# Optimization experiments

Measured on AMD Instinct MI355X. Metric: run time of the kernel, lower is better.

Reference implementation:

```python
import jax, jax.numpy as jnp
import numpy as np

B, N, CH, DIM, SLOTS, ITERS, HID = 32, 4096, 256, 256, 11, 3, 512
EPS_ATTN = 1e-8
LN_EPS = 1e-3


def _ln(x, g, b):
    m = jnp.mean(x, axis=-1, keepdims=True)
    v = jnp.mean((x - m) ** 2, axis=-1, keepdims=True)
    return (x - m) * jax.lax.rsqrt(v + LN_EPS) * g + b


def setup_inputs() -> dict:
    key = jax.random.key(0)
    ks = jax.random.split(key, 16)
    s = lambda d: 1.0 / np.sqrt(d)
    return {
        "inputs": jax.random.normal(ks[0], (B, N, CH), jnp.float32),
        "noise": jax.random.normal(ks[1], (B, SLOTS, DIM), jnp.float32),
        "slots_mu": jax.random.uniform(ks[2], (1, 1, DIM), jnp.float32, -0.15, 0.15),
        "slots_log_sigma": jax.random.uniform(ks[3], (1, 1, DIM), jnp.float32, -0.15, 0.15),
        "Wq": jax.random.normal(ks[4], (DIM, DIM), jnp.float32) * s(DIM),
        "Wk": jax.random.normal(ks[5], (DIM, CH), jnp.float32) * s(CH),
        "Wv": jax.random.normal(ks[6], (DIM, CH), jnp.float32) * s(CH),
        "W_ih": jax.random.normal(ks[7], (3 * DIM, DIM), jnp.float32) * s(DIM),
        "W_hh": jax.random.normal(ks[8], (3 * DIM, DIM), jnp.float32) * s(DIM),
        "b_ih": jnp.zeros((3 * DIM,), jnp.float32),
        "b_hh": jnp.zeros((3 * DIM,), jnp.float32),
        "W1": jax.random.normal(ks[9], (HID, DIM), jnp.float32) * s(DIM),
        "b1": jnp.zeros((HID,), jnp.float32),
        "W2": jax.random.normal(ks[10], (DIM, HID), jnp.float32) * s(HID),
        "b2": jnp.zeros((DIM,), jnp.float32),
        "g_in": jnp.ones((CH,), jnp.float32), "be_in": jnp.zeros((CH,), jnp.float32),
        "g_sl": jnp.ones((DIM,), jnp.float32), "be_sl": jnp.zeros((DIM,), jnp.float32),
        "g_ff": jnp.ones((DIM,), jnp.float32), "be_ff": jnp.zeros((DIM,), jnp.float32),
    }


def reference(inputs, noise, slots_mu, slots_log_sigma, Wq, Wk, Wv, W_ih, W_hh,
              b_ih, b_hh, W1, b1, W2, b2, g_in, be_in, g_sl, be_sl, g_ff, be_ff):
    scale = DIM ** -0.5
    # reparameterized slot init: Normal(mu, exp(log_sigma))
    slots = slots_mu + jnp.exp(slots_log_sigma) * noise  # (B, S, D)
    x = _ln(inputs, g_in, be_in)
    k = jnp.einsum('bnc,dc->bnd', x, Wk)  # (B, N, D)
    v = jnp.einsum('bnc,dc->bnd', x, Wv)

    def gru(u, h):
        gi = u @ W_ih.T + b_ih
        gh = h @ W_hh.T + b_hh
        i_r, i_z, i_n = jnp.split(gi, 3, axis=-1)
        h_r, h_z, h_n = jnp.split(gh, 3, axis=-1)
        r = jax.nn.sigmoid(i_r + h_r)
        z = jax.nn.sigmoid(i_z + h_z)
        n = jnp.tanh(i_n + r * h_n)
        return (1.0 - z) * n + z * h

    for _ in range(ITERS):
        slots_prev = slots
        q = jnp.einsum('bid,ed->bie', _ln(slots, g_sl, be_sl), Wq)
        dots = jnp.einsum('bid,bjd->bij', q, k) * scale  # (B, S, N)
        attn = jax.nn.softmax(dots, axis=1) + EPS_ATTN   # competitive over slots
        attn = attn / jnp.sum(attn, axis=-1, keepdims=True)
        updates = jnp.einsum('bjd,bij->bid', v, attn)    # (B, S, D)
        slots = gru(updates.reshape(-1, DIM), slots_prev.reshape(-1, DIM)).reshape(B, -1, DIM)
        h = jax.nn.relu(_ln(slots, g_ff, be_ff) @ W1.T + b1)
        slots = slots + h @ W2.T + b2
    return slots
```

## Files before the change

### kernel.cpp

```cpp
#include <hip/hip_runtime.h>
#include <hip/hip_bf16.h>
#include <math.h>

typedef __bf16 bf16;
typedef __bf16 bf16x4 __attribute__((ext_vector_type(4)));
typedef __bf16 bf16x8 __attribute__((ext_vector_type(8)));
typedef float  f32x4  __attribute__((ext_vector_type(4)));

#define DEVI static __device__ __forceinline__

constexpr int B_ = 32, N_ = 4096, NS_ = 11, SP_ = 16, ITERS_ = 3;
constexpr int P_ = 32;
constexpr float LN_EPS_ = 1e-3f;
constexpr float EPS_ATTN_ = 1e-8f;

DEVI f32x4 mfma16(bf16x8 a, bf16x8 b, f32x4 c) {
  return __builtin_amdgcn_mfma_f32_16x16x32_bf16(a, b, c, 0, 0, 0);
}

DEVI float wsum64(float v) {
#pragma unroll
  for (int m = 32; m > 0; m >>= 1) v += __shfl_xor(v, m, 64);
  return v;
}

__global__ __launch_bounds__(256) void cast_weights(
    const float* __restrict__ Wq, const float* __restrict__ Wk,
    const float* __restrict__ Wv, const float* __restrict__ Wih,
    const float* __restrict__ Whh, const float* __restrict__ W1,
    const float* __restrict__ W2,
    bf16* __restrict__ cWkT, bf16* __restrict__ cWvT, bf16* __restrict__ cWq,
    bf16* __restrict__ cWih, bf16* __restrict__ cWhh, bf16* __restrict__ cW1,
    bf16* __restrict__ cW2) {
  const int idx = blockIdx.x * 256 + threadIdx.x;
  const int n0 = 256 * 256;
  const int n1 = n0 + 256 * 256;
  const int n2 = n1 + 256 * 256;
  const int n3 = n2 + 768 * 256;
  const int n4 = n3 + 768 * 256;
  const int n5 = n4 + 512 * 256;
  const int n6 = n5 + 256 * 512;
  if (idx < n0) {
    const int c = idx >> 8, d = idx & 255;
    cWkT[idx] = (bf16)Wk[d * 256 + c];
  } else if (idx < n1) {
    const int i = idx - n0; const int c = i >> 8, d = i & 255;
    cWvT[i] = (bf16)Wv[d * 256 + c];
  } else if (idx < n2) { const int i = idx - n1; cWq[i]  = (bf16)Wq[i];
  } else if (idx < n3) { const int i = idx - n2; cWih[i] = (bf16)Wih[i];
  } else if (idx < n4) { const int i = idx - n3; cWhh[i] = (bf16)Whh[i];
  } else if (idx < n5) { const int i = idx - n4; cW1[i]  = (bf16)W1[i];
  } else if (idx < n6) { const int i = idx - n5; cW2[i]  = (bf16)W2[i]; }
}

__global__ __launch_bounds__(256) void wfold_gemm(
    const bf16* __restrict__ Wih, const bf16* __restrict__ WvT,
    bf16* __restrict__ Wfold) {
  __shared__ bf16 At[32 * 256];
  const int mt = blockIdx.x, nt = blockIdx.y;
  const int tid = threadIdx.x, lane = tid & 63, wid = tid >> 6;
  const int l15 = lane & 15, gq = lane >> 4;
  const bf16* A = Wih + (size_t)mt * 32 * 256;
#pragma unroll
  for (int i = 0; i < 4; ++i) {
    const int idx = i * 256 + tid, row = idx >> 5, c = idx & 31;
    const bf16x8 v = *(const bf16x8*)(A + row * 256 + c * 8);
    const int byte = (row * 512 + c * 16) ^ ((row & 7) << 4);
    *(bf16x8*)((char*)At + byte) = v;
  }
  __syncthreads();
  const int wr = wid >> 1, wc = wid & 1;
  f32x4 acc[2] = {};
  for (int kk = 0; kk < 8; ++kk) {
    const int arow = wr * 16 + l15;
    const int byte = (arow * 512 + kk * 64 + gq * 16) ^ ((arow & 7) << 4);
    const bf16x8 af = *(const bf16x8*)((const char*)At + byte);
#pragma unroll
    for (int nn = 0; nn < 2; ++nn) {
      const bf16* wrow = WvT + (size_t)(nt * 64 + wc * 32 + nn * 16 + l15) * 256 + kk * 32 + gq * 8;
      acc[nn] = mfma16(af, *(const bf16x8*)wrow, acc[nn]);
    }
  }
#pragma unroll
  for (int nn = 0; nn < 2; ++nn)
#pragma unroll
    for (int r = 0; r < 4; ++r) {
      const int grow = mt * 32 + wr * 16 + gq * 4 + r;
      const int col = nt * 64 + wc * 32 + nn * 16 + l15;
      Wfold[(size_t)grow * 256 + col] = (bf16)acc[nn][r];
    }
}

__global__ __launch_bounds__(256) void init_slots(
    const float* __restrict__ mu, const float* __restrict__ lsig,
    const float* __restrict__ noise, float* __restrict__ slots,
    bf16* __restrict__ slots_bf) {
  const int idx = blockIdx.x * 256 + threadIdx.x;
  const int d = idx & 255;
  const float v = mu[d] + expf(lsig[d]) * noise[idx];
  slots[idx] = v;
  slots_bf[idx] = (bf16)v;
}

__global__ __launch_bounds__(256) void ln_cast(
    const float* __restrict__ inp, const float* __restrict__ g,
    const float* __restrict__ be, bf16* __restrict__ xhat) {
  const int tid = threadIdx.x, lane = tid & 63, wid = tid >> 6;
  const int l15 = lane & 15, gq = lane >> 4;
  float4 gv[4], bv4[4];
#pragma unroll
  for (int u = 0; u < 4; ++u) {
    gv[u]  = ((const float4*)g)[l15 * 4 + u];
    bv4[u] = ((const float4*)be)[l15 * 4 + u];
  }
  const int nwaves = gridDim.x * 4;
  const int gw = blockIdx.x * 4 + wid;
  for (int qi = gw; qi < (B_ * N_ / 4); qi += nwaves) {
    const size_t grow = (size_t)qi * 4 + gq;
    const float4* rp = (const float4*)(inp + grow * 256 + l15 * 16);
    float4 x[4];
#pragma unroll
    for (int u = 0; u < 4; ++u) x[u] = rp[u];
    float s = 0.f, ss = 0.f;
#pragma unroll
    for (int u = 0; u < 4; ++u) {
      s += x[u].x + x[u].y + x[u].z + x[u].w;
      ss = fmaf(x[u].x, x[u].x, fmaf(x[u].y, x[u].y,
           fmaf(x[u].z, x[u].z, fmaf(x[u].w, x[u].w, ss))));
    }
#pragma unroll
    for (int m = 8; m > 0; m >>= 1) {
      s  += __shfl_xor(s,  m, 16);
      ss += __shfl_xor(ss, m, 16);
    }
    const float mean = s * (1.f / 256.f);
    const float rstd = rsqrtf(ss * (1.f / 256.f) - mean * mean + LN_EPS_);
    bf16x8 y0, y1;
#pragma unroll
    for (int u = 0; u < 2; ++u) {
      y0[u * 4 + 0] = (bf16)((x[u].x - mean) * rstd * gv[u].x + bv4[u].x);
      y0[u * 4 + 1] = (bf16)((x[u].y - mean) * rstd * gv[u].y + bv4[u].y);
      y0[u * 4 + 2] = (bf16)((x[u].z - mean) * rstd * gv[u].z + bv4[u].z);
      y0[u * 4 + 3] = (bf16)((x[u].w - mean) * rstd * gv[u].w + bv4[u].w);
      y1[u * 4 + 0] = (bf16)((x[2+u].x - mean) * rstd * gv[2+u].x + bv4[2+u].x);
      y1[u * 4 + 1] = (bf16)((x[2+u].y - mean) * rstd * gv[2+u].y + bv4[2+u].y);
      y1[u * 4 + 2] = (bf16)((x[2+u].z - mean) * rstd * gv[2+u].z + bv4[2+u].z);
      y1[u * 4 + 3] = (bf16)((x[2+u].w - mean) * rstd * gv[2+u].w + bv4[2+u].w);
    }
    bf16* orow = xhat + grow * 256 + l15 * 16;
    *(bf16x8*)orow       = y0;
    *(bf16x8*)(orow + 8) = y1;
  }
}

__global__ __launch_bounds__(256) void q_proj(
    const float* __restrict__ slots, const float* __restrict__ g,
    const float* __restrict__ be, const bf16* __restrict__ Wqb,
    const bf16* __restrict__ WkT, bf16* __restrict__ qpad) {
  const int i = blockIdx.x, b = blockIdx.y, t = threadIdx.x;
  bf16* out = qpad + (b * SP_ + i) * 256;
  if (i >= NS_) { out[t] = (bf16)0.f; return; }
  __shared__ float lnv[256], qd[256];
  __shared__ float red[8];
  const float x = slots[(b * NS_ + i) * 256 + t];
  float s = wsum64(x), ss = wsum64(x * x);
  const int lane = t & 63, w = t >> 6;
  if (lane == 0) { red[w] = s; red[4 + w] = ss; }
  __syncthreads();
  const float st = red[0] + red[1] + red[2] + red[3];
  const float qt = red[4] + red[5] + red[6] + red[7];
  const float mean = st / 256.f, var = qt / 256.f - mean * mean;
  const float rstd = rsqrtf(var + LN_EPS_);
  lnv[t] = (x - mean) * rstd * g[t] + be[t];
  __syncthreads();
  {
    float acc = 0.f;
    const bf16* wr = Wqb + (size_t)t * 256;
    for (int it = 0; it < 32; ++it) {
      const bf16x8 wv = *(const bf16x8*)(wr + it * 8);
      const float* u = &lnv[it * 8];
#pragma unroll
      for (int e = 0; e < 8; ++e) acc += (float)wv[e] * u[e];
    }
    qd[t] = acc;
  }
  __syncthreads();
  {
    float acc = 0.f;
    const bf16* wr = WkT + (size_t)t * 256;
    for (int it = 0; it < 32; ++it) {
      const bf16x8 wv = *(const bf16x8*)(wr + it * 8);
      const float* u = &qd[it * 8];
#pragma unroll
      for (int e = 0; e < 8; ++e) acc += (float)wv[e] * u[e];
    }
    out[t] = (bf16)(acc * 0.0625f);
  }
}

__global__ __launch_bounds__(256) void attn_part(
    const bf16* __restrict__ xhat, const bf16* __restrict__ qpad,
    bf16* __restrict__ num_part, float* __restrict__ den_part) {
  const int part = blockIdx.x, b = blockIdx.y;
  const int lane = threadIdx.x & 63, wid = threadIdx.x >> 6;
  const int l15 = lane & 15, gq = lane >> 4;
  const int jbase = part * 128 + wid * 32;
  const bf16* qrow = qpad + ((size_t)(b * SP_ + l15)) * 256;
  const bf16* kbase = xhat + ((size_t)(b * N_ + jbase)) * 256;
  __shared__ bf16 vlds[4][4096];
  __shared__ float nsw[2][4096];
  __shared__ float dens[4][16];
  char* myv = (char*)&vlds[wid][0];
  const int srow = gq;

  bf16x8 vst[8];
#pragma unroll
  for (int i = 0; i < 8; ++i)
    vst[i] = *(const bf16x8*)(kbase + (size_t)(i * 4 + srow) * 256 + l15 * 8);
  bf16x8 bq[8];
#pragma unroll
  for (int kk = 0; kk < 8; ++kk)
    bq[kk] = *(const bf16x8*)(qrow + kk * 32 + gq * 8);

  float denacc = 0.f;
  float p0[4], p1[4];
#pragma unroll
  for (int T = 0; T < 2; ++T) {
    const bf16* krow = kbase + (size_t)(T * 16 + l15) * 256;
    f32x4 d = {0.f, 0.f, 0.f, 0.f};
#pragma unroll
    for (int kk = 0; kk < 8; ++kk) {
      const bf16x8 ak = *(const bf16x8*)(krow + kk * 32 + gq * 8);
      d = mfma16(ak, bq[kk], d);
    }
#pragma unroll
    for (int r = 0; r < 4; ++r) {
      float vmax = (l15 < NS_) ? d[r] : -1e30f;
#pragma unroll
      for (int mm = 8; mm > 0; mm >>= 1) vmax = fmaxf(vmax, __shfl_xor(vmax, mm, 16));
      const float e = (l15 < NS_) ? expf(d[r] - vmax) : 0.f;
      float ssum = e;
#pragma unroll
      for (int mm = 8; mm > 0; mm >>= 1) ssum += __shfl_xor(ssum, mm, 16);
      const float p = (l15 < NS_) ? (e / ssum + EPS_ATTN_) : 0.f;
      if (T == 0) p0[r] = p; else p1[r] = p;
      denacc += p;
    }
  }
  bf16x8 ap;
#pragma unroll
  for (int e = 0; e < 8; ++e) {
    const int srcl = l15 + ((2 * (gq & 1) + (e >> 2)) << 4);
    const float va = __shfl(p0[e & 3], srcl, 64);
    const float vb = __shfl(p1[e & 3], srcl, 64);
    ap[e] = (bf16)((gq < 2) ? va : vb);
  }
  f32x4 accN[16];
#pragma unroll
  for (int i = 0; i < 8; ++i) {
    const int row = i * 4 + srow;
    const int byte = (row * 256 + l15 * 16) ^ ((((row >> 3) & 3)) << 5);
    *(bf16x8*)(myv + byte) = vst[i];
  }
#pragma unroll
  for (int i = 0; i < 8; ++i)
    vst[i] = *(const bf16x8*)(kbase + (size_t)(i * 4 + srow) * 256 + 128 + l15 * 8);
  __builtin_amdgcn_s_setprio(1);
#pragma unroll
  for (int l = 0; l < 8; ++l) {
    bf16x8 bvf;
#pragma unroll
    for (int e = 0; e < 8; ++e) {
      const int row = 8 * gq + e;
      const int byte = (row * 256 + l * 32 + l15 * 2) ^ ((((row >> 3) & 3)) << 5);
      bvf[e] = *(const bf16*)(myv + byte);
    }
    f32x4 z = {0.f, 0.f, 0.f, 0.f};
    accN[l] = mfma16(ap, bvf, z);
  }
  __builtin_amdgcn_s_setprio(0);
#pragma unroll
  for (int i = 0; i < 8; ++i) {
    const int row = i * 4 + srow;
    const int byte = (row * 256 + l15 * 16) ^ ((((row >> 3) & 3)) << 5);
    *(bf16x8*)(myv + byte) = vst[i];
  }
  __builtin_amdgcn_s_setprio(1);
#pragma unroll
  for (int l = 0; l < 8; ++l) {
    bf16x8 bvf;
#pragma unroll
    for (int e = 0; e < 8; ++e) {
      const int row = 8 * gq + e;
      const int byte = (row * 256 + l * 32 + l15 * 2) ^ ((((row >> 3) & 3)) << 5);
      bvf[e] = *(const bf16*)(myv + byte);
    }
    f32x4 z = {0.f, 0.f, 0.f, 0.f};
    accN[8 + l] = mfma16(ap, bvf, z);
  }
  __builtin_amdgcn_s_setprio(0);
  if (wid < 2) {
#pragma unroll
    for (int dblk = 0; dblk < 16; ++dblk)
#pragma unroll
      for (int r = 0; r < 4; ++r) {
        const int idx = (((4 * gq + r) * 256) + dblk * 16 + l15) ^ (gq << 4);
        nsw[wid][idx] = accN[dblk][r];
      }
  }
  __syncthreads();
  if (wid >= 2) {
#pragma unroll
    for (int dblk = 0; dblk < 16; ++dblk)
#pragma unroll
      for (int r = 0; r < 4; ++r) {
        const int idx = (((4 * gq + r) * 256) + dblk * 16 + l15) ^ (gq << 4);
        nsw[wid - 2][idx] += accN[dblk][r];
      }
  }
  float dtot = denacc + __shfl_xor(denacc, 16, 64);
  dtot += __shfl_xor(dtot, 32, 64);
  if (lane < 16) dens[wid][l15] = dtot;
  __syncthreads();
  const int t = threadIdx.x;
  if (t < NS_)
    den_part[(b * P_ + part) * NS_ + t] =
        dens[0][t] + dens[1][t] + dens[2][t] + dens[3][t];
  for (int r = 0; r < NS_; ++r) {
    const int swz = ((r >> 2) & 3) << 4;
    num_part[((size_t)((b * P_ + part) * NS_ + r)) * 256 + t] =
        (bf16)(nsw[0][(r * 256 + t) ^ swz] + nsw[1][(r * 256 + t) ^ swz]);
  }
}

__global__ __launch_bounds__(256) void u0_reduce(
    const bf16* __restrict__ num_part, const float* __restrict__ den_part,
    bf16* __restrict__ u0b) {
  const int row = blockIdx.x, t = threadIdx.x;
  const int b = row / NS_, i = row % NS_;
  float nsum = 0.f;
  for (int p = 0; p < P_; ++p)
    nsum += (float)num_part[((size_t)((b * P_ + p) * NS_ + i)) * 256 + t];
  float den = 0.f;
  for (int p = 0; p < P_; ++p) den += den_part[(b * P_ + p) * NS_ + i];
  u0b[(size_t)row * 256 + t] = (bf16)(nsum / den);
}

__global__ __launch_bounds__(256) void gates_gemm(
    const bf16* __restrict__ u0b, const bf16* __restrict__ hb,
    const bf16* __restrict__ Wfold, const bf16* __restrict__ Whh,
    float* __restrict__ gi, float* __restrict__ gh) {
  __shared__ bf16 At[32 * 256];
  const int mt = blockIdx.x, nt = blockIdx.y;
  const bool isI = nt < 12;
  const int ntile = isI ? nt : nt - 12;
  const bf16* A = (isI ? u0b : hb) + (size_t)mt * 32 * 256;
  const bf16* W = isI ? Wfold : Whh;
  float* out = isI ? gi : gh;
  const int tid = threadIdx.x, lane = tid & 63, wid = tid >> 6;
  const int l15 = lane & 15, gq = lane >> 4;
#pragma unroll
  for (int i = 0; i < 4; ++i) {
    const int idx = i * 256 + tid, row = idx >> 5, c = idx & 31;
    const bf16x8 v = *(const bf16x8*)(A + row * 256 + c * 8);
    const int byte = (row * 512 + c * 16) ^ ((row & 7) << 4);
    *(bf16x8*)((char*)At + byte) = v;
  }
  __syncthreads();
  const int wr = wid >> 1, wc = wid & 1;
  f32x4 acc[2] = {};
  for (int kk = 0; kk < 8; ++kk) {
    const int arow = wr * 16 + l15;
    const int byte = (arow * 512 + kk * 64 + gq * 16) ^ ((arow & 7) << 4);
    const bf16x8 af = *(const bf16x8*)((const char*)At + byte);
#pragma unroll
    for (int nn = 0; nn < 2; ++nn) {
      const bf16* wrow = W + (size_t)(ntile * 64 + wc * 32 + nn * 16 + l15) * 256 + kk * 32 + gq * 8;
      acc[nn] = mfma16(af, *(const bf16x8*)wrow, acc[nn]);
    }
  }
#pragma unroll
  for (int nn = 0; nn < 2; ++nn)
#pragma unroll
    for (int r = 0; r < 4; ++r) {
      const int grow = mt * 32 + wr * 16 + gq * 4 + r;
      const int col = ntile * 64 + wc * 32 + nn * 16 + l15;
      out[(size_t)grow * 768 + col] = acc[nn][r];
    }
}

__global__ __launch_bounds__(256) void gru_ew(
    const float* __restrict__ gi, const float* __restrict__ gh,
    const float* __restrict__ bih, const float* __restrict__ bhh,
    const float* __restrict__ slots_f, const float* __restrict__ gff,
    const float* __restrict__ beff, float* __restrict__ hn_out,
    bf16* __restrict__ ln_out) {
  const int row = blockIdx.x, t = threadIdx.x;
  __shared__ float red[8];
  const size_t g0 = (size_t)row * 768;
  const float ir = gi[g0 + t]       + bih[t];
  const float hr = gh[g0 + t]       + bhh[t];
  const float iz = gi[g0 + 256 + t] + bih[256 + t];
  const float hz = gh[g0 + 256 + t] + bhh[256 + t];
  const float inn = gi[g0 + 512 + t] + bih[512 + t];
  const float hnn = gh[g0 + 512 + t] + bhh[512 + t];
  const float h = slots_f[(size_t)row * 256 + t];
  const float r = 1.f / (1.f + expf(-(ir + hr)));
  const float z = 1.f / (1.f + expf(-(iz + hz)));
  const float n = tanhf(inn + r * hnn);
  const float hn = (1.f - z) * n + z * h;
  hn_out[(size_t)row * 256 + t] = hn;
  float s = wsum64(hn), ss = wsum64(hn * hn);
  const int lane = t & 63, w = t >> 6;
  if (lane == 0) { red[w] = s; red[4 + w] = ss; }
  __syncthreads();
  const float st = red[0] + red[1] + red[2] + red[3];
  const float qt = red[4] + red[5] + red[6] + red[7];
  const float mean = st / 256.f, var = qt / 256.f - mean * mean;
  const float rstd = rsqrtf(var + LN_EPS_);
  ln_out[(size_t)row * 256 + t] = (bf16)((hn - mean) * rstd * gff[t] + beff[t]);
}

__global__ __launch_bounds__(256) void w1_gemm(
    const bf16* __restrict__ lnb, const bf16* __restrict__ W1,
    const float* __restrict__ b1, bf16* __restrict__ h1b) {
  __shared__ bf16 At[32 * 256];
  const int mt = blockIdx.x, nt = blockIdx.y;
  const int tid = threadIdx.x, lane = tid & 63, wid = tid >> 6;
  const int l15 = lane & 15, gq = lane >> 4;
  const bf16* A = lnb + (size_t)mt * 32 * 256;
#pragma unroll
  for (int i = 0; i < 4; ++i) {
    const int idx = i * 256 + tid, row = idx >> 5, c = idx & 31;
    const bf16x8 v = *(const bf16x8*)(A + row * 256 + c * 8);
    const int byte = (row * 512 + c * 16) ^ ((row & 7) << 4);
    *(bf16x8*)((char*)At + byte) = v;
  }
  __syncthreads();
  const int wr = wid >> 1, wc = wid & 1;
  f32x4 acc[2] = {};
  for (int kk = 0; kk < 8; ++kk) {
    const int arow = wr * 16 + l15;
    const int byte = (arow * 512 + kk * 64 + gq * 16) ^ ((arow & 7) << 4);
    const bf16x8 af = *(const bf16x8*)((const char*)At + byte);
#pragma unroll
    for (int nn = 0; nn < 2; ++nn) {
      const bf16* wrow = W1 + (size_t)(nt * 64 + wc * 32 + nn * 16 + l15) * 256 + kk * 32 + gq * 8;
      acc[nn] = mfma16(af, *(const bf16x8*)wrow, acc[nn]);
    }
  }
#pragma unroll
  for (int nn = 0; nn < 2; ++nn)
#pragma unroll
    for (int r = 0; r < 4; ++r) {
      const int grow = mt * 32 + wr * 16 + gq * 4 + r;
      const int col = nt * 64 + wc * 32 + nn * 16 + l15;
      h1b[(size_t)grow * 512 + col] = (bf16)fmaxf(acc[nn][r] + b1[col], 0.f);
    }
}

__global__ __launch_bounds__(256) void w2_gemm(
    const bf16* __restrict__ h1b, const bf16* __restrict__ W2,
    const float* __restrict__ b2, const float* __restrict__ hn_in,
    float* __restrict__ sout, bf16* __restrict__ sbf) {
  __shared__ bf16 At[32 * 512];
  const int mt = blockIdx.x, nt = blockIdx.y;
  const int tid = threadIdx.x, lane = tid & 63, wid = tid >> 6;
  const int l15 = lane & 15, gq = lane >> 4;
  const bf16* A = h1b + (size_t)mt * 32 * 512;
#pragma unroll
  for (int i = 0; i < 8; ++i) {
    const int idx = i * 256 + tid, row = idx >> 6, c = idx & 63;
    const bf16x8 v = *(const bf16x8*)(A + row * 512 + c * 8);
    const int byte = (row * 1024 + c * 16) ^ ((row & 7) << 4);
    *(bf16x8*)((char*)At + byte) = v;
  }
  __syncthreads();
  const int wr = wid >> 1, wc = wid & 1;
  f32x4 acc[2] = {};
  for (int kk = 0; kk < 16; ++kk) {
    const int arow = wr * 16 + l15;
    const int byte = (arow * 1024 + kk * 64 + gq * 16) ^ ((arow & 7) << 4);
    const bf16x8 af = *(const bf16x8*)((const char*)At + byte);
#pragma unroll
    for (int nn = 0; nn < 2; ++nn) {
      const bf16* wrow = W2 + (size_t)(nt * 64 + wc * 32 + nn * 16 + l15) * 512 + kk * 32 + gq * 8;
      acc[nn] = mfma16(af, *(const bf16x8*)wrow, acc[nn]);
    }
  }
#pragma unroll
  for (int nn = 0; nn < 2; ++nn)
#pragma unroll
    for (int r = 0; r < 4; ++r) {
      const int grow = mt * 32 + wr * 16 + gq * 4 + r;
      const int col = nt * 64 + wc * 32 + nn * 16 + l15;
      const float v = hn_in[(size_t)grow * 256 + col] + acc[nn][r] + b2[col];
      sout[(size_t)grow * 256 + col] = v;
      sbf[(size_t)grow * 256 + col] = (bf16)v;
    }
}

extern "C" void kernel_launch(void* const* d_in, const int* in_sizes, int n_in,
                              void* d_out, int out_size, void* d_ws, size_t ws_size,
                              hipStream_t stream) {
  const float* inputs = (const float*)d_in[0];
  const float* noise  = (const float*)d_in[1];
  const float* mu     = (const float*)d_in[2];
  const float* lsig   = (const float*)d_in[3];
  const float* Wq     = (const float*)d_in[4];
  const float* Wk     = (const float*)d_in[5];
  const float* Wv     = (const float*)d_in[6];
  const float* Wih    = (const float*)d_in[7];
  const float* Whh    = (const float*)d_in[8];
  const float* bih    = (const float*)d_in[9];
  const float* bhh    = (const float*)d_in[10];
  const float* W1     = (const float*)d_in[11];
  const float* b1     = (const float*)d_in[12];
  const float* W2     = (const float*)d_in[13];
  const float* b2     = (const float*)d_in[14];
  const float* gin    = (const float*)d_in[15];
  const float* bein   = (const float*)d_in[16];
  const float* gsl    = (const float*)d_in[17];
  const float* besl   = (const float*)d_in[18];
  const float* gff    = (const float*)d_in[19];
  const float* beff   = (const float*)d_in[20];

  char* ws = (char*)d_ws;
  size_t off = 0;
  auto alloc = [&](size_t bytes) -> void* {
    void* p = ws + off;
    off += (bytes + 255) & ~(size_t)255;
    return p;
  };
  bf16*  xhat    = (bf16*) alloc((size_t)B_ * N_ * 256 * 2);
  bf16*  qpad    = (bf16*) alloc((size_t)B_ * SP_ * 256 * 2);
  bf16*  cWkT    = (bf16*) alloc(256 * 256 * 2);
  bf16*  cWvT    = (bf16*) alloc(256 * 256 * 2);
  bf16*  cWq     = (bf16*) alloc(256 * 256 * 2);
  bf16*  cWih    = (bf16*) alloc(768 * 256 * 2);
  bf16*  cWhh    = (bf16*) alloc(768 * 256 * 2);
  bf16*  cW1     = (bf16*) alloc(512 * 256 * 2);
  bf16*  cW2     = (bf16*) alloc(256 * 512 * 2);
  bf16*  Wfold   = (bf16*) alloc(768 * 256 * 2);
  float* slots   = (float*)alloc((size_t)352 * 256 * 4);
  bf16*  slots_bf= (bf16*) alloc((size_t)352 * 256 * 2);
  bf16*  numpart = (bf16*) alloc((size_t)B_ * P_ * NS_ * 256 * 2);
  float* denpart = (float*)alloc((size_t)B_ * P_ * NS_ * 4);
  bf16*  u0b     = (bf16*) alloc((size_t)352 * 256 * 2);
  float* gi      = (float*)alloc((size_t)352 * 768 * 4);
  float* gh      = (float*)alloc((size_t)352 * 768 * 4);
  float* hn_f    = (float*)alloc((size_t)352 * 256 * 4);
  bf16*  ln_b    = (bf16*) alloc((size_t)352 * 256 * 2);
  bf16*  h1b     = (bf16*) alloc((size_t)352 * 512 * 2);
  (void)ws_size; (void)in_sizes; (void)n_in; (void)out_size;

  cast_weights<<<3328, 256, 0, stream>>>(Wq, Wk, Wv, Wih, Whh, W1, W2,
                                         cWkT, cWvT, cWq, cWih, cWhh, cW1, cW2);
  wfold_gemm<<<dim3(24, 4), 256, 0, stream>>>(cWih, cWvT, Wfold);
  init_slots<<<352, 256, 0, stream>>>(mu, lsig, noise, slots, slots_bf);
  ln_cast<<<2048, 256, 0, stream>>>(inputs, gin, bein, xhat);
  for (int it = 0; it < ITERS_; ++it) {
    q_proj<<<dim3(SP_, B_), 256, 0, stream>>>(slots, gsl, besl, cWq, cWkT, qpad);
    attn_part<<<dim3(P_, B_), 256, 0, stream>>>(xhat, qpad, numpart, denpart);
    u0_reduce<<<352, 256, 0, stream>>>(numpart, denpart, u0b);
    gates_gemm<<<dim3(11, 24), 256, 0, stream>>>(u0b, slots_bf, Wfold, cWhh, gi, gh);
    gru_ew<<<352, 256, 0, stream>>>(gi, gh, bih, bhh, slots, gff, beff, hn_f, ln_b);
    w1_gemm<<<dim3(11, 8), 256, 0, stream>>>(ln_b, cW1, b1, h1b);
    float* sout = (it == ITERS_ - 1) ? (float*)d_out : slots;
    w2_gemm<<<dim3(11, 4), 256, 0, stream>>>(h1b, cW2, b2, hn_f, sout, slots_bf);
  }
}
```

Baseline: 263.8 us.

## Fuse GRU gate GEMMs with elementwise update and LayerNorm into W1 load

Merges the gate GEMM and GRU elementwise kernel into one kernel that computes all three gates for both input and hidden paths per column tile, then applies the GRU directly from accumulators. The feed-forward LayerNorm moves into the W1 GEMM's tile load, removing one launch and the gi/gh/ln intermediate buffers per iteration. The attention partial-sum LDS buffer also drops from fp32 to bf16, halving its shared memory to raise occupancy at the cost of precision. The fused gates kernel uses fewer blocks (44 vs 264) and the W1 blocks redo the LayerNorm for each column tile.

```diff
diff --git a/kernel.cpp b/kernel.cpp
--- a/kernel.cpp
+++ b/kernel.cpp
@@ -208,7 +208,7 @@
   const bf16* qrow = qpad + ((size_t)(b * SP_ + l15)) * 256;
   const bf16* kbase = xhat + ((size_t)(b * N_ + jbase)) * 256;
   __shared__ bf16 vlds[4][4096];
-  __shared__ float nsw[2][4096];
+  __shared__ bf16 nsw[2][4096];
   __shared__ float dens[4][16];
   char* myv = (char*)&vlds[wid][0];
   const int srow = gq;
@@ -305,7 +305,7 @@
 #pragma unroll
       for (int r = 0; r < 4; ++r) {
         const int idx = (((4 * gq + r) * 256) + dblk * 16 + l15) ^ (gq << 4);
-        nsw[wid][idx] = accN[dblk][r];
+        nsw[wid][idx] = (bf16)accN[dblk][r];
       }
   }
   __syncthreads();
@@ -315,7 +315,7 @@
 #pragma unroll
       for (int r = 0; r < 4; ++r) {
         const int idx = (((4 * gq + r) * 256) + dblk * 16 + l15) ^ (gq << 4);
-        nsw[wid - 2][idx] += accN[dblk][r];
+        nsw[wid - 2][idx] = (bf16)((float)nsw[wid - 2][idx] + accN[dblk][r]);
       }
   }
   float dtot = denacc + __shfl_xor(denacc, 16, 64);
@@ -329,7 +329,7 @@
   for (int r = 0; r < NS_; ++r) {
     const int swz = ((r >> 2) & 3) << 4;
     num_part[((size_t)((b * P_ + part) * NS_ + r)) * 256 + t] =
-        (bf16)(nsw[0][(r * 256 + t) ^ swz] + nsw[1][(r * 256 + t) ^ swz]);
+        (bf16)((float)nsw[0][(r * 256 + t) ^ swz] + (float)nsw[1][(r * 256 + t) ^ swz]);
   }
 }
 
@@ -346,95 +346,101 @@
   u0b[(size_t)row * 256 + t] = (bf16)(nsum / den);
 }
 
-__global__ __launch_bounds__(256) void gates_gemm(
+__global__ __launch_bounds__(256) void gates_ew(
     const bf16* __restrict__ u0b, const bf16* __restrict__ hb,
     const bf16* __restrict__ Wfold, const bf16* __restrict__ Whh,
-    float* __restrict__ gi, float* __restrict__ gh) {
-  __shared__ bf16 At[32 * 256];
+    const float* __restrict__ bih, const float* __restrict__ bhh,
+    const float* __restrict__ slots_f, float* __restrict__ hn_out) {
+  __shared__ bf16 Au[32 * 256];
+  __shared__ bf16 Ah[32 * 256];
   const int mt = blockIdx.x, nt = blockIdx.y;
-  const bool isI = nt < 12;
-  const int ntile = isI ? nt : nt - 12;
-  const bf16* A = (isI ? u0b : hb) + (size_t)mt * 32 * 256;
-  const bf16* W = isI ? Wfold : Whh;
-  float* out = isI ? gi : gh;
   const int tid = threadIdx.x, lane = tid & 63, wid = tid >> 6;
   const int l15 = lane & 15, gq = lane >> 4;
 #pragma unroll
   for (int i = 0; i < 4; ++i) {
     const int idx = i * 256 + tid, row = idx >> 5, c = idx & 31;
-    const bf16x8 v = *(const bf16x8*)(A + row * 256 + c * 8);
     const int byte = (row * 512 + c * 16) ^ ((row & 7) << 4);
-    *(bf16x8*)((char*)At + byte) = v;
+    *(bf16x8*)((char*)Au + byte) =
+        *(const bf16x8*)(u0b + (size_t)(mt * 32 + row) * 256 + c * 8);
+    *(bf16x8*)((char*)Ah + byte) =
+        *(const bf16x8*)(hb + (size_t)(mt * 32 + row) * 256 + c * 8);
   }
   __syncthreads();
   const int wr = wid >> 1, wc = wid & 1;
-  f32x4 acc[2] = {};
+  f32x4 ai[3][2] = {}, ah[3][2] = {};
   for (int kk = 0; kk < 8; ++kk) {
     const int arow = wr * 16 + l15;
     const int byte = (arow * 512 + kk * 64 + gq * 16) ^ ((arow & 7) << 4);
-    const bf16x8 af = *(const bf16x8*)((const char*)At + byte);
-#pragma unroll
-    for (int nn = 0; nn < 2; ++nn) {
-      const bf16* wrow = W + (size_t)(ntile * 64 + wc * 32 + nn * 16 + l15) * 256 + kk * 32 + gq * 8;
-      acc[nn] = mfma16(af, *(const bf16x8*)wrow, acc[nn]);
-    }
-  }
-#pragma unroll
-  for (int nn = 0; nn < 2; ++nn)
+    const bf16x8 au = *(const bf16x8*)((const char*)Au + byte);
+    const bf16x8 av = *(const bf16x8*)((const char*)Ah + byte);
+#pragma unroll
+    for (int ggt = 0; ggt < 3; ++ggt)
+#pragma unroll
+      for (int tc = 0; tc < 2; ++tc) {
+        const size_t wrow = (size_t)(ggt * 256 + nt * 64 + wc * 32 + tc * 16 + l15) * 256 + kk * 32 + gq * 8;
+        ai[ggt][tc] = mfma16(au, *(const bf16x8*)(Wfold + wrow), ai[ggt][tc]);
+        ah[ggt][tc] = mfma16(av, *(const bf16x8*)(Whh + wrow), ah[ggt][tc]);
+      }
+  }
+#pragma unroll
+  for (int tc = 0; tc < 2; ++tc) {
+    const int col = nt * 64 + wc * 32 + tc * 16 + l15;
+    const float bir = bih[col],        bhr = bhh[col];
+    const float biz = bih[256 + col],  bhz = bhh[256 + col];
+    const float bin = bih[512 + col],  bhn = bhh[512 + col];
 #pragma unroll
     for (int r = 0; r < 4; ++r) {
       const int grow = mt * 32 + wr * 16 + gq * 4 + r;
-      const int col = ntile * 64 + wc * 32 + nn * 16 + l15;
-      out[(size_t)grow * 768 + col] = acc[nn][r];
-    }
-}
-
-__global__ __launch_bounds__(256) void gru_ew(
-    const float* __restrict__ gi, const float* __restrict__ gh,
-    const float* __restrict__ bih, const float* __restrict__ bhh,
-    const float* __restrict__ slots_f, const float* __restrict__ gff,
-    const float* __restrict__ beff, float* __restrict__ hn_out,
-    bf16* __restrict__ ln_out) {
-  const int row = blockIdx.x, t = threadIdx.x;
-  __shared__ float red[8];
-  const size_t g0 = (size_t)row * 768;
-  const float ir = gi[g0 + t]       + bih[t];
-  const float hr = gh[g0 + t]       + bhh[t];
-  const float iz = gi[g0 + 256 + t] + bih[256 + t];
-  const float hz = gh[g0 + 256 + t] + bhh[256 + t];
-  const float inn = gi[g0 + 512 + t] + bih[512 + t];
-  const float hnn = gh[g0 + 512 + t] + bhh[512 + t];
-  const float h = slots_f[(size_t)row * 256 + t];
-  const float r = 1.f / (1.f + expf(-(ir + hr)));
-  const float z = 1.f / (1.f + expf(-(iz + hz)));
-  const float n = tanhf(inn + r * hnn);
-  const float hn = (1.f - z) * n + z * h;
-  hn_out[(size_t)row * 256 + t] = hn;
-  float s = wsum64(hn), ss = wsum64(hn * hn);
-  const int lane = t & 63, w = t >> 6;
-  if (lane == 0) { red[w] = s; red[4 + w] = ss; }
-  __syncthreads();
-  const float st = red[0] + red[1] + red[2] + red[3];
-  const float qt = red[4] + red[5] + red[6] + red[7];
-  const float mean = st / 256.f, var = qt / 256.f - mean * mean;
-  const float rstd = rsqrtf(var + LN_EPS_);
-  ln_out[(size_t)row * 256 + t] = (bf16)((hn - mean) * rstd * gff[t] + beff[t]);
+      const float ir = ai[0][tc][r] + bir, hr = ah[0][tc][r] + bhr;
+      const float iz = ai[1][tc][r] + biz, hz = ah[1][tc][r] + bhz;
+      const float inn = ai[2][tc][r] + bin, hnn = ah[2][tc][r] + bhn;
+      const float h = slots_f[(size_t)grow * 256 + col];
+      const float rg = 1.f / (1.f + expf(-(ir + hr)));
+      const float zg = 1.f / (1.f + expf(-(iz + hz)));
+      const float ng = tanhf(inn + rg * hnn);
+      hn_out[(size_t)grow * 256 + col] = (1.f - zg) * ng + zg * h;
+    }
+  }
 }
 
 __global__ __launch_bounds__(256) void w1_gemm(
-    const bf16* __restrict__ lnb, const bf16* __restrict__ W1,
+    const float* __restrict__ hn_f, const float* __restrict__ gff,
+    const float* __restrict__ beff, const bf16* __restrict__ W1,
     const float* __restrict__ b1, bf16* __restrict__ h1b) {
   __shared__ bf16 At[32 * 256];
   const int mt = blockIdx.x, nt = blockIdx.y;
   const int tid = threadIdx.x, lane = tid & 63, wid = tid >> 6;
   const int l15 = lane & 15, gq = lane >> 4;
-  const bf16* A = lnb + (size_t)mt * 32 * 256;
 #pragma unroll
   for (int i = 0; i < 4; ++i) {
     const int idx = i * 256 + tid, row = idx >> 5, c = idx & 31;
-    const bf16x8 v = *(const bf16x8*)(A + row * 256 + c * 8);
+    const float* src = hn_f + (size_t)(mt * 32 + row) * 256 + c * 8;
+    const float4 f0 = ((const float4*)src)[0];
+    const float4 f1 = ((const float4*)src)[1];
+    float s  = f0.x + f0.y + f0.z + f0.w + f1.x + f1.y + f1.z + f1.w;
+    float ss = fmaf(f0.x, f0.x, fmaf(f0.y, f0.y, fmaf(f0.z, f0.z,
+               fmaf(f0.w, f0.w, fmaf(f1.x, f1.x, fmaf(f1.y, f1.y,
+               fmaf(f1.z, f1.z, f1.w * f1.w)))))));
+#pragma unroll
+    for (int m = 16; m > 0; m >>= 1) {
+      s  += __shfl_xor(s,  m, 32);
+      ss += __shfl_xor(ss, m, 32);
+    }
+    const float mean = s * (1.f / 256.f);
+    const float rstd = rsqrtf(ss * (1.f / 256.f) - mean * mean + LN_EPS_);
+    bf16x8 y;
+    const float* gp = gff + c * 8;
+    const float* bp = beff + c * 8;
+    y[0] = (bf16)((f0.x - mean) * rstd * gp[0] + bp[0]);
+    y[1] = (bf16)((f0.y - mean) * rstd * gp[1] + bp[1]);
+    y[2] = (bf16)((f0.z - mean) * rstd * gp[2] + bp[2]);
+    y[3] = (bf16)((f0.w - mean) * rstd * gp[3] + bp[3]);
+    y[4] = (bf16)((f1.x - mean) * rstd * gp[4] + bp[4]);
+    y[5] = (bf16)((f1.y - mean) * rstd * gp[5] + bp[5]);
+    y[6] = (bf16)((f1.z - mean) * rstd * gp[6] + bp[6]);
+    y[7] = (bf16)((f1.w - mean) * rstd * gp[7] + bp[7]);
     const int byte = (row * 512 + c * 16) ^ ((row & 7) << 4);
-    *(bf16x8*)((char*)At + byte) = v;
+    *(bf16x8*)((char*)At + byte) = y;
   }
   __syncthreads();
   const int wr = wid >> 1, wc = wid & 1;
@@ -547,10 +553,7 @@
   bf16*  numpart = (bf16*) alloc((size_t)B_ * P_ * NS_ * 256 * 2);
   float* denpart = (float*)alloc((size_t)B_ * P_ * NS_ * 4);
   bf16*  u0b     = (bf16*) alloc((size_t)352 * 256 * 2);
-  float* gi      = (float*)alloc((size_t)352 * 768 * 4);
-  float* gh      = (float*)alloc((size_t)352 * 768 * 4);
   float* hn_f    = (float*)alloc((size_t)352 * 256 * 4);
-  bf16*  ln_b    = (bf16*) alloc((size_t)352 * 256 * 2);
   bf16*  h1b     = (bf16*) alloc((size_t)352 * 512 * 2);
   (void)ws_size; (void)in_sizes; (void)n_in; (void)out_size;
 
@@ -563,9 +566,9 @@
     q_proj<<<dim3(SP_, B_), 256, 0, stream>>>(slots, gsl, besl, cWq, cWkT, qpad);
     attn_part<<<dim3(P_, B_), 256, 0, stream>>>(xhat, qpad, numpart, denpart);
     u0_reduce<<<352, 256, 0, stream>>>(numpart, denpart, u0b);
-    gates_gemm<<<dim3(11, 24), 256, 0, stream>>>(u0b, slots_bf, Wfold, cWhh, gi, gh);
-    gru_ew<<<352, 256, 0, stream>>>(gi, gh, bih, bhh, slots, gff, beff, hn_f, ln_b);
-    w1_gemm<<<dim3(11, 8), 256, 0, stream>>>(ln_b, cW1, b1, h1b);
+    gates_ew<<<dim3(11, 4), 256, 0, stream>>>(u0b, slots_bf, Wfold, cWhh,
+                                              bih, bhh, slots, hn_f);
+    w1_gemm<<<dim3(11, 8), 256, 0, stream>>>(hn_f, gff, beff, cW1, b1, h1b);
     float* sout = (it == ITERS_ - 1) ? (float*)d_out : slots;
     w2_gemm<<<dim3(11, 4), 256, 0, stream>>>(h1b, cW2, b2, hn_f, sout, slots_bf);
   }
```

Measured after the change: 312.2 us. 18.4% more time.
